# Kernel optimization log

Hardware: AMD Instinct MI355X
Metric: run time of the kernel (lower is better)

The kernel has to match this reference:

```python
import jax, jax.numpy as jnp
import numpy as np

VALUE_SCALE = 0.1  # paper: values ~ N(0, (0.1*std)^2); weights are unit-std here


def setup_inputs() -> dict:
    key = jax.random.key(0)
    k1, k2, k3, k4 = jax.random.split(key, 4)
    O, I = 4096, 4096
    n_flip = 1_000_000
    x = jax.random.normal(k1, (256, I), dtype=jnp.float32)
    weight = jax.random.normal(k2, (O, I), dtype=jnp.float32)
    prune_mask = jax.random.uniform(k3, (O, I)) < 0.6
    weight = jnp.where(prune_mask, 0.0, weight)
    flip_idx = jax.random.randint(k4, (n_flip,), 0, O * I, dtype=jnp.int64)
    values = jax.random.normal(jax.random.fold_in(key, 7), (n_flip,), dtype=jnp.float32)
    return {"x": x, "weight": weight, "flip_idx": flip_idx, "values": values}


def reference(x, weight, flip_idx, values):
    # 'restore' mode: scatter small random values into pruned weight positions
    # (single fused scatter instead of a python loop of scalar writes),
    # then run the wrapped model's forward (Linear without bias).
    O, I = weight.shape
    w_flat = weight.reshape(-1)
    w_mod = w_flat.at[flip_idx].set(values * VALUE_SCALE).reshape(O, I)
    # y = x @ W^T  -- [B, I] x [O, I] -> [B, O]
    return jnp.einsum('bi,oi->bo', x, w_mod)
```

## Files before the change

### kernel.cpp

```cpp
#include <hip/hip_runtime.h>
#include <hip/hip_bf16.h>
#include <stdint.h>
#include <stddef.h>

#define BATCH 256
#define OC 4096
#define IC 4096
#define VALUE_SCALE 0.1f

#define BN 64
#define BK 32
#define KS 8
#define KPER (IC / KS)
#define NT (KPER / BK)
#define YSZ (BATCH * OC)

typedef float f32x4 __attribute__((ext_vector_type(4)));
typedef int   i32x4 __attribute__((ext_vector_type(4)));
typedef short bf16x8 __attribute__((ext_vector_type(8)));

__global__ void scatter_k(float* __restrict__ w, const int* __restrict__ idx,
                          const float* __restrict__ val, int n) {
    int i = (blockIdx.x * blockDim.x + threadIdx.x) * 4;
    if (i + 4 <= n) {
        i32x4 id = *(const i32x4*)(idx + i);
        f32x4 v  = *(const f32x4*)(val + i);
        w[id[0]] = v[0] * VALUE_SCALE;
        w[id[1]] = v[1] * VALUE_SCALE;
        w[id[2]] = v[2] * VALUE_SCALE;
        w[id[3]] = v[3] * VALUE_SCALE;
    } else {
        for (int j = i; j < n; ++j) w[idx[j]] = val[j] * VALUE_SCALE;
    }
}

__device__ __forceinline__ void gload16(const float* src, float* ldsDst) {
    __builtin_amdgcn_global_load_lds(
        (const __attribute__((address_space(1))) void*)src,
        (__attribute__((address_space(3))) void*)ldsDst, 16, 0, 0);
}

__device__ __forceinline__ short f2bf_rn(float f) {
    return (short)__bfloat16_as_ushort(__float2bfloat16(f));
}

__global__ __launch_bounds__(256, 2) void gemm_k(const float* __restrict__ x,
                                                 const float* __restrict__ w,
                                                 float* __restrict__ part,
                                                 float* __restrict__ y) {
    const int tid  = threadIdx.x;
    const int lane = tid & 63;
    const int wv   = tid >> 6;
    const int bid  = blockIdx.x;
    const int ks   = bid & 7;
    const int bn   = bid >> 3;
    const int k0   = ks * KPER;
    const int nc0  = bn * BN;

    __shared__ __align__(16) float At[2][BATCH * BK];
    __shared__ __align__(16) float Bt[2][BN * BK];

    f32x4 acc[4][4];
#pragma unroll
    for (int m = 0; m < 4; ++m)
#pragma unroll
        for (int n = 0; n < 4; ++n) acc[m][n] = (f32x4)0.0f;

    auto stage = [&](int buf, int t) {
        const int kg = k0 + t * BK;
        const int rsub = lane >> 3;
        const int csl  = lane & 7;
#pragma unroll
        for (int j = 0; j < 8; ++j) {
            int r0  = wv * 64 + j * 8;
            int row = r0 + rsub;
            int c   = csl ^ (row & 7);
            gload16(x + (size_t)row * IC + kg + c * 4, &At[buf][r0 * BK]);
        }
#pragma unroll
        for (int j = 0; j < 2; ++j) {
            int r0  = wv * 16 + j * 8;
            int row = r0 + rsub;
            int c   = csl ^ (row & 7);
            gload16(w + (size_t)(nc0 + row) * IC + kg + c * 4, &Bt[buf][r0 * BK]);
        }
    };

    auto readFrag = [&](const float* tile, int row) -> bf16x8 {
        int c0  = (lane >> 4) * 2;
        int cp0 = c0 ^ (row & 7);
        int cp1 = (c0 + 1) ^ (row & 7);
        const float* base = tile + row * BK;
        f32x4 lo = *(const f32x4*)(base + cp0 * 4);
        f32x4 hi = *(const f32x4*)(base + cp1 * 4);
        bf16x8 r;
#pragma unroll
        for (int j = 0; j < 4; ++j) {
            r[j]     = f2bf_rn(lo[j]);
            r[j + 4] = f2bf_rn(hi[j]);
        }
        return r;
    };

    stage(0, 0);
    __syncthreads();

    for (int t = 0; t < NT; ++t) {
        const int cur = t & 1;
        if (t + 1 < NT) stage(cur ^ 1, t + 1);

        bf16x8 a[4], b[4];
#pragma unroll
        for (int m = 0; m < 4; ++m)
            a[m] = readFrag(At[cur], wv * 64 + m * 16 + (lane & 15));
#pragma unroll
        for (int n = 0; n < 4; ++n)
            b[n] = readFrag(Bt[cur], n * 16 + (lane & 15));
#pragma unroll
        for (int n = 0; n < 4; ++n)
#pragma unroll
            for (int m = 0; m < 4; ++m)
                acc[m][n] = __builtin_amdgcn_mfma_f32_16x16x32_bf16(a[m], b[n], acc[m][n], 0, 0, 0);

        __syncthreads();
    }

    if (part) {
        float* dst = part + (size_t)ks * YSZ;
#pragma unroll
        for (int m = 0; m < 4; ++m) {
            int r0 = wv * 64 + m * 16 + (lane >> 4) * 4;
#pragma unroll
            for (int n = 0; n < 4; ++n) {
                int c = nc0 + n * 16 + (lane & 15);
#pragma unroll
                for (int r = 0; r < 4; ++r)
                    dst[(size_t)(r0 + r) * OC + c] = acc[m][n][r];
            }
        }
    } else {
#pragma unroll
        for (int m = 0; m < 4; ++m) {
            int r0 = wv * 64 + m * 16 + (lane >> 4) * 4;
#pragma unroll
            for (int n = 0; n < 4; ++n) {
                int c = nc0 + n * 16 + (lane & 15);
#pragma unroll
                for (int r = 0; r < 4; ++r)
                    atomicAdd(&y[(size_t)(r0 + r) * OC + c], acc[m][n][r]);
            }
        }
    }
}

__global__ void reduce_k(const float* __restrict__ part, float* __restrict__ y) {
    int i = (blockIdx.x * blockDim.x + threadIdx.x) * 4;
    f32x4 s = *(const f32x4*)(part + i);
#pragma unroll
    for (int p = 1; p < KS; ++p) s += *(const f32x4*)(part + (size_t)p * YSZ + i);
    *(f32x4*)(y + i) = s;
}

extern "C" void kernel_launch(void* const* d_in, const int* in_sizes, int n_in,
                              void* d_out, int out_size, void* d_ws, size_t ws_size,
                              hipStream_t stream) {
    const float* x  = (const float*)d_in[0];
    float*       w  = (float*)d_in[1];
    const int*   fi = (const int*)d_in[2];
    const float* fv = (const float*)d_in[3];
    float*       y  = (float*)d_out;
    const int nflip = in_sizes[2];

    const bool use_ws = ws_size >= (size_t)KS * YSZ * sizeof(float);
    float* part = use_ws ? (float*)d_ws : nullptr;

    if (!use_ws) hipMemsetAsync(d_out, 0, (size_t)out_size * sizeof(float), stream);
    scatter_k<<<dim3((nflip + 1023) / 1024), dim3(256), 0, stream>>>(w, fi, fv, nflip);
    gemm_k<<<dim3((OC / BN) * KS), dim3(256), 0, stream>>>(x, w, part, y);
    if (use_ws)
        reduce_k<<<dim3(YSZ / (4 * 256)), dim3(256), 0, stream>>>(part, y);
}
```

Measured before the change: 152.5 us.

## Bin flip scatter by row range and stage GEMM tiles as bf16 in LDS

Replaces the direct random scatter with a two-pass scheme: a binning kernel groups flip pairs into 256 buckets by high index bits, then a replay kernel writes each bucket so that stores hit a localized region of the weight matrix. The GEMM now loads fp32 tiles into registers, converts them to bf16 once, and writes them to a swizzled bf16 LDS buffer, instead of DMAing fp32 into LDS and converting on every fragment read. This halves LDS footprint and removes the repeated conversions, and it drops the launch-bounds occupancy hint. The binning path overwrites the start of the workspace that is also used for partial sums, but the GEMM runs afterwards so there is no conflict. Bucket overflow past BINCAP would silently drop writes, and duplicate-index ordering across bins may differ from the reference.

```diff
diff --git a/kernel.cpp b/kernel.cpp
--- a/kernel.cpp
+++ b/kernel.cpp
@@ -15,39 +15,79 @@
 #define NT (KPER / BK)
 #define YSZ (BATCH * OC)
 
+#define NBIN 256
+#define BINCAP 8192
+#define BIN_ELEMS 4096
+
 typedef float f32x4 __attribute__((ext_vector_type(4)));
-typedef int   i32x4 __attribute__((ext_vector_type(4)));
 typedef short bf16x8 __attribute__((ext_vector_type(8)));
+
+__device__ __forceinline__ short f2bf(float f) {
+    return (short)__bfloat16_as_ushort(__float2bfloat16(f));
+}
+
+__device__ __forceinline__ void barrier_nodrain() {
+    asm volatile("s_waitcnt lgkmcnt(0)" ::: "memory");
+    __builtin_amdgcn_sched_barrier(0);
+    __builtin_amdgcn_s_barrier();
+    __builtin_amdgcn_sched_barrier(0);
+}
+
+__global__ void bin_k(const int* __restrict__ idx, const float* __restrict__ val, int n,
+                      int* __restrict__ gcnt, int2* __restrict__ pairs) {
+    __shared__ int hcnt[NBIN];
+    __shared__ int hbase[NBIN];
+    const int t = threadIdx.x;
+    for (int b = t; b < NBIN; b += 256) hcnt[b] = 0;
+    __syncthreads();
+
+    const int start = blockIdx.x * BIN_ELEMS;
+    int mi[16]; float mv[16]; int mp[16];
+#pragma unroll
+    for (int e = 0; e < 16; ++e) {
+        int i = start + e * 256 + t;
+        if (i < n) {
+            mi[e] = idx[i];
+            mv[e] = val[i];
+            mp[e] = atomicAdd(&hcnt[mi[e] >> 16], 1);
+        }
+    }
+    __syncthreads();
+    for (int b = t; b < NBIN; b += 256)
+        if (hcnt[b] > 0) hbase[b] = atomicAdd(&gcnt[b], hcnt[b]);
+    __syncthreads();
+#pragma unroll
+    for (int e = 0; e < 16; ++e) {
+        int i = start + e * 256 + t;
+        if (i < n) {
+            int bin = mi[e] >> 16;
+            int pos = hbase[bin] + mp[e];
+            if (pos < BINCAP)
+                pairs[(size_t)bin * BINCAP + pos] = make_int2(mi[e], __float_as_int(mv[e]));
+        }
+    }
+}
+
+__global__ void replay_k(const int* __restrict__ gcnt, const int2* __restrict__ pairs,
+                         float* __restrict__ w) {
+    const int b = blockIdx.x;
+    int cnt = gcnt[b]; if (cnt > BINCAP) cnt = BINCAP;
+    for (int i = threadIdx.x; i < cnt; i += 256) {
+        int2 p = pairs[(size_t)b * BINCAP + i];
+        w[p.x] = __int_as_float(p.y) * VALUE_SCALE;
+    }
+}
 
 __global__ void scatter_k(float* __restrict__ w, const int* __restrict__ idx,
                           const float* __restrict__ val, int n) {
-    int i = (blockIdx.x * blockDim.x + threadIdx.x) * 4;
-    if (i + 4 <= n) {
-        i32x4 id = *(const i32x4*)(idx + i);
-        f32x4 v  = *(const f32x4*)(val + i);
-        w[id[0]] = v[0] * VALUE_SCALE;
-        w[id[1]] = v[1] * VALUE_SCALE;
-        w[id[2]] = v[2] * VALUE_SCALE;
-        w[id[3]] = v[3] * VALUE_SCALE;
-    } else {
-        for (int j = i; j < n; ++j) w[idx[j]] = val[j] * VALUE_SCALE;
-    }
-}
-
-__device__ __forceinline__ void gload16(const float* src, float* ldsDst) {
-    __builtin_amdgcn_global_load_lds(
-        (const __attribute__((address_space(1))) void*)src,
-        (__attribute__((address_space(3))) void*)ldsDst, 16, 0, 0);
-}
-
-__device__ __forceinline__ short f2bf_rn(float f) {
-    return (short)__bfloat16_as_ushort(__float2bfloat16(f));
-}
-
-__global__ __launch_bounds__(256, 2) void gemm_k(const float* __restrict__ x,
-                                                 const float* __restrict__ w,
-                                                 float* __restrict__ part,
-                                                 float* __restrict__ y) {
+    int i = blockIdx.x * blockDim.x + threadIdx.x;
+    if (i < n) w[idx[i]] = val[i] * VALUE_SCALE;
+}
+
+__global__ __launch_bounds__(256) void gemm_k(const float* __restrict__ x,
+                                              const float* __restrict__ w,
+                                              float* __restrict__ part,
+                                              float* __restrict__ y) {
     const int tid  = threadIdx.x;
     const int lane = tid & 63;
     const int wv   = tid >> 6;
@@ -57,8 +97,8 @@
     const int k0   = ks * KPER;
     const int nc0  = bn * BN;
 
-    __shared__ __align__(16) float At[2][BATCH * BK];
-    __shared__ __align__(16) float Bt[2][BN * BK];
+    __shared__ __align__(16) short At[2][BATCH * BK];
+    __shared__ __align__(16) short Bt[2][BN * BK];
 
     f32x4 acc[4][4];
 #pragma unroll
@@ -66,63 +106,80 @@
 #pragma unroll
         for (int n = 0; n < 4; ++n) acc[m][n] = (f32x4)0.0f;
 
-    auto stage = [&](int buf, int t) {
-        const int kg = k0 + t * BK;
-        const int rsub = lane >> 3;
-        const int csl  = lane & 7;
-#pragma unroll
-        for (int j = 0; j < 8; ++j) {
-            int r0  = wv * 64 + j * 8;
-            int row = r0 + rsub;
-            int c   = csl ^ (row & 7);
-            gload16(x + (size_t)row * IC + kg + c * 4, &At[buf][r0 * BK]);
-        }
-#pragma unroll
-        for (int j = 0; j < 2; ++j) {
-            int r0  = wv * 16 + j * 8;
-            int row = r0 + rsub;
-            int c   = csl ^ (row & 7);
-            gload16(w + (size_t)(nc0 + row) * IC + kg + c * 4, &Bt[buf][r0 * BK]);
+    f32x4 ra[8];
+    f32x4 rb[2];
+
+    const int rsub = lane >> 2;
+    const int csl  = lane & 3;
+
+    auto load_regs = [&](int t) {
+        const int kg = k0 + t * BK + csl * 8;
+#pragma unroll
+        for (int j = 0; j < 4; ++j) {
+            const float* s = x + (size_t)(wv * 64 + j * 16 + rsub) * IC + kg;
+            ra[2 * j]     = *(const f32x4*)s;
+            ra[2 * j + 1] = *(const f32x4*)(s + 4);
+        }
+        {
+            const float* s = w + (size_t)(nc0 + wv * 16 + rsub) * IC + kg;
+            rb[0] = *(const f32x4*)s;
+            rb[1] = *(const f32x4*)(s + 4);
         }
     };
 
-    auto readFrag = [&](const float* tile, int row) -> bf16x8 {
-        int c0  = (lane >> 4) * 2;
-        int cp0 = c0 ^ (row & 7);
-        int cp1 = (c0 + 1) ^ (row & 7);
-        const float* base = tile + row * BK;
-        f32x4 lo = *(const f32x4*)(base + cp0 * 4);
-        f32x4 hi = *(const f32x4*)(base + cp1 * 4);
-        bf16x8 r;
+    auto write_lds = [&](int buf) {
 #pragma unroll
         for (int j = 0; j < 4; ++j) {
-            r[j]     = f2bf_rn(lo[j]);
-            r[j + 4] = f2bf_rn(hi[j]);
-        }
-        return r;
+            int row = wv * 64 + j * 16 + rsub;
+            bf16x8 v;
+#pragma unroll
+            for (int q = 0; q < 4; ++q) { v[q] = f2bf(ra[2 * j][q]); v[q + 4] = f2bf(ra[2 * j + 1][q]); }
+            int csw = csl ^ ((row >> 1) & 3);
+            *(bf16x8*)&At[buf][row * BK + csw * 8] = v;
+        }
+        {
+            int row = wv * 16 + rsub;
+            bf16x8 v;
+#pragma unroll
+            for (int q = 0; q < 4; ++q) { v[q] = f2bf(rb[0][q]); v[q + 4] = f2bf(rb[1][q]); }
+            int csw = csl ^ ((row >> 1) & 3);
+            *(bf16x8*)&Bt[buf][row * BK + csw * 8] = v;
+        }
     };
 
-    stage(0, 0);
-    __syncthreads();
+    auto compute = [&](int buf) {
+        bf16x8 a[4], b[4];
+        const int cs = lane >> 4;
+#pragma unroll
+        for (int m = 0; m < 4; ++m) {
+            int row = wv * 64 + m * 16 + (lane & 15);
+            a[m] = *(const bf16x8*)&At[buf][row * BK + (cs ^ ((row >> 1) & 3)) * 8];
+        }
+#pragma unroll
+        for (int n = 0; n < 4; ++n) {
+            int row = n * 16 + (lane & 15);
+            b[n] = *(const bf16x8*)&Bt[buf][row * BK + (cs ^ ((row >> 1) & 3)) * 8];
+        }
+#pragma unroll
+        for (int n = 0; n < 4; ++n)
+#pragma unroll
+            for (int m = 0; m < 4; ++m)
+                acc[m][n] = __builtin_amdgcn_mfma_f32_16x16x32_bf16(a[m], b[n], acc[m][n], 0, 0, 0);
+    };
+
+    load_regs(0);
+    write_lds(0);
+    barrier_nodrain();
 
     for (int t = 0; t < NT; ++t) {
         const int cur = t & 1;
-        if (t + 1 < NT) stage(cur ^ 1, t + 1);
-
-        bf16x8 a[4], b[4];
-#pragma unroll
-        for (int m = 0; m < 4; ++m)
-            a[m] = readFrag(At[cur], wv * 64 + m * 16 + (lane & 15));
-#pragma unroll
-        for (int n = 0; n < 4; ++n)
-            b[n] = readFrag(Bt[cur], n * 16 + (lane & 15));
-#pragma unroll
-        for (int n = 0; n < 4; ++n)
-#pragma unroll
-            for (int m = 0; m < 4; ++m)
-                acc[m][n] = __builtin_amdgcn_mfma_f32_16x16x32_bf16(a[m], b[n], acc[m][n], 0, 0, 0);
-
-        __syncthreads();
+        if (t + 1 < NT) load_regs(t + 1);
+        compute(cur);
+        barrier_nodrain();
+        if (t + 1 < NT) {
+            write_lds(cur ^ 1);
+            barrier_nodrain();
+        }
     }
 
     if (part) {
@@ -174,8 +231,16 @@
     const bool use_ws = ws_size >= (size_t)KS * YSZ * sizeof(float);
     float* part = use_ws ? (float*)d_ws : nullptr;
 
-    if (!use_ws) hipMemsetAsync(d_out, 0, (size_t)out_size * sizeof(float), stream);
-    scatter_k<<<dim3((nflip + 1023) / 1024), dim3(256), 0, stream>>>(w, fi, fv, nflip);
+    if (use_ws) {
+        int*  gcnt  = (int*)d_ws;
+        int2* pairs = (int2*)((char*)d_ws + 4096);
+        hipMemsetAsync(gcnt, 0, NBIN * sizeof(int), stream);
+        bin_k<<<dim3((nflip + BIN_ELEMS - 1) / BIN_ELEMS), dim3(256), 0, stream>>>(fi, fv, nflip, gcnt, pairs);
+        replay_k<<<dim3(NBIN), dim3(256), 0, stream>>>(gcnt, pairs, w);
+    } else {
+        hipMemsetAsync(d_out, 0, (size_t)out_size * sizeof(float), stream);
+        scatter_k<<<dim3((nflip + 255) / 256), dim3(256), 0, stream>>>(w, fi, fv, nflip);
+    }
     gemm_k<<<dim3((OC / BN) * KS), dim3(256), 0, stream>>>(x, w, part, y);
     if (use_ws)
         reduce_k<<<dim3(YSZ / (4 * 256)), dim3(256), 0, stream>>>(part, y);
```

Measured after the change: 163.3 us. +7.1%, slower.

## Load GEMM operands directly into registers instead of staging through LDS

Applied to the files above, without the earlier changes.

Removes the shared-memory double buffer and barriers. Each wave now loads its A rows and all B rows straight from global memory into registers, prefetching the next K tile while converting the current one to bf16. This eliminates LDS writes and reads and the __syncthreads per tile. In exchange, the W tile is fetched four times per block (once per wave) instead of being shared, and register usage grows.

```diff
diff --git a/kernel.cpp b/kernel.cpp
--- a/kernel.cpp
+++ b/kernel.cpp
@@ -19,6 +19,10 @@
 typedef int   i32x4 __attribute__((ext_vector_type(4)));
 typedef short bf16x8 __attribute__((ext_vector_type(8)));
 
+__device__ __forceinline__ short f2bf(float f) {
+    return (short)__bfloat16_as_ushort(__float2bfloat16(f));
+}
+
 __global__ void scatter_k(float* __restrict__ w, const int* __restrict__ idx,
                           const float* __restrict__ val, int n) {
     int i = (blockIdx.x * blockDim.x + threadIdx.x) * 4;
@@ -34,16 +38,6 @@
     }
 }
 
-__device__ __forceinline__ void gload16(const float* src, float* ldsDst) {
-    __builtin_amdgcn_global_load_lds(
-        (const __attribute__((address_space(1))) void*)src,
-        (__attribute__((address_space(3))) void*)ldsDst, 16, 0, 0);
-}
-
-__device__ __forceinline__ short f2bf_rn(float f) {
-    return (short)__bfloat16_as_ushort(__float2bfloat16(f));
-}
-
 __global__ __launch_bounds__(256, 2) void gemm_k(const float* __restrict__ x,
                                                  const float* __restrict__ w,
                                                  float* __restrict__ part,
@@ -57,8 +51,11 @@
     const int k0   = ks * KPER;
     const int nc0  = bn * BN;
 
-    __shared__ __align__(16) float At[2][BATCH * BK];
-    __shared__ __align__(16) float Bt[2][BN * BK];
+    const int r = lane & 15;
+    const int q = lane >> 4;
+
+    const float* xbase = x + (size_t)(wv * 64 + r) * IC + k0 + q * 8;
+    const float* wbase = w + (size_t)(nc0 + r)     * IC + k0 + q * 8;
 
     f32x4 acc[4][4];
 #pragma unroll
@@ -66,63 +63,47 @@
 #pragma unroll
         for (int n = 0; n < 4; ++n) acc[m][n] = (f32x4)0.0f;
 
-    auto stage = [&](int buf, int t) {
-        const int kg = k0 + t * BK;
-        const int rsub = lane >> 3;
-        const int csl  = lane & 7;
+    f32x4 ra[8], rb[8];
+    bf16x8 fa[4], fb[4];
+
+    auto loadRaw = [&](int t) {
+        const int ko = t * BK;
 #pragma unroll
-        for (int j = 0; j < 8; ++j) {
-            int r0  = wv * 64 + j * 8;
-            int row = r0 + rsub;
-            int c   = csl ^ (row & 7);
-            gload16(x + (size_t)row * IC + kg + c * 4, &At[buf][r0 * BK]);
+        for (int m = 0; m < 4; ++m) {
+            const float* s = xbase + (size_t)m * 16 * IC + ko;
+            ra[2 * m]     = *(const f32x4*)s;
+            ra[2 * m + 1] = *(const f32x4*)(s + 4);
         }
 #pragma unroll
-        for (int j = 0; j < 2; ++j) {
-            int r0  = wv * 16 + j * 8;
-            int row = r0 + rsub;
-            int c   = csl ^ (row & 7);
-            gload16(w + (size_t)(nc0 + row) * IC + kg + c * 4, &Bt[buf][r0 * BK]);
+        for (int n = 0; n < 4; ++n) {
+            const float* s = wbase + (size_t)n * 16 * IC + ko;
+            rb[2 * n]     = *(const f32x4*)s;
+            rb[2 * n + 1] = *(const f32x4*)(s + 4);
         }
     };
 
-    auto readFrag = [&](const float* tile, int row) -> bf16x8 {
-        int c0  = (lane >> 4) * 2;
-        int cp0 = c0 ^ (row & 7);
-        int cp1 = (c0 + 1) ^ (row & 7);
-        const float* base = tile + row * BK;
-        f32x4 lo = *(const f32x4*)(base + cp0 * 4);
-        f32x4 hi = *(const f32x4*)(base + cp1 * 4);
-        bf16x8 r;
+    auto cvtAll = [&]() {
 #pragma unroll
-        for (int j = 0; j < 4; ++j) {
-            r[j]     = f2bf_rn(lo[j]);
-            r[j + 4] = f2bf_rn(hi[j]);
+        for (int m = 0; m < 4; ++m) {
+#pragma unroll
+            for (int j = 0; j < 4; ++j) {
+                fa[m][j]     = f2bf(ra[2 * m][j]);
+                fa[m][j + 4] = f2bf(ra[2 * m + 1][j]);
+                fb[m][j]     = f2bf(rb[2 * m][j]);
+                fb[m][j + 4] = f2bf(rb[2 * m + 1][j]);
+            }
         }
-        return r;
     };
 
-    stage(0, 0);
-    __syncthreads();
-
+    loadRaw(0);
     for (int t = 0; t < NT; ++t) {
-        const int cur = t & 1;
-        if (t + 1 < NT) stage(cur ^ 1, t + 1);
-
-        bf16x8 a[4], b[4];
-#pragma unroll
-        for (int m = 0; m < 4; ++m)
-            a[m] = readFrag(At[cur], wv * 64 + m * 16 + (lane & 15));
-#pragma unroll
-        for (int n = 0; n < 4; ++n)
-            b[n] = readFrag(Bt[cur], n * 16 + (lane & 15));
+        cvtAll();
+        if (t + 1 < NT) loadRaw(t + 1);
 #pragma unroll
         for (int n = 0; n < 4; ++n)
 #pragma unroll
             for (int m = 0; m < 4; ++m)
-                acc[m][n] = __builtin_amdgcn_mfma_f32_16x16x32_bf16(a[m], b[n], acc[m][n], 0, 0, 0);
-
-        __syncthreads();
+                acc[m][n] = __builtin_amdgcn_mfma_f32_16x16x32_bf16(fa[m], fb[n], acc[m][n], 0, 0, 0);
     }
 
     if (part) {
@@ -134,8 +115,8 @@
             for (int n = 0; n < 4; ++n) {
                 int c = nc0 + n * 16 + (lane & 15);
 #pragma unroll
-                for (int r = 0; r < 4; ++r)
-                    dst[(size_t)(r0 + r) * OC + c] = acc[m][n][r];
+                for (int rr = 0; rr < 4; ++rr)
+                    dst[(size_t)(r0 + rr) * OC + c] = acc[m][n][rr];
             }
         }
     } else {
@@ -146,8 +127,8 @@
             for (int n = 0; n < 4; ++n) {
                 int c = nc0 + n * 16 + (lane & 15);
 #pragma unroll
-                for (int r = 0; r < 4; ++r)
-                    atomicAdd(&y[(size_t)(r0 + r) * OC + c], acc[m][n][r]);
+                for (int rr = 0; rr < 4; ++rr)
+                    atomicAdd(&y[(size_t)(r0 + rr) * OC + c], acc[m][n][rr]);
             }
         }
     }
```

Result: slower. 173.2 us (+13.5%).
